# Optimization experiments

Measured on AMD Instinct MI355X. Metric: run time of the kernel, lower is better.

Reference implementation:

```python
import jax, jax.numpy as jnp
from jax import lax
import numpy as np

DN = ('NCHW', 'OIHW', 'NCHW')
EPS = 1e-8
LRELU_SLOPE = 0.2
SQRT2 = np.float32(np.sqrt(2.0))


def _blur2d(x):
    # 5x5 binomial FIR, depthwise, padding=2, stride=1 (Blur2d(kernel_size=5, padding=2))
    k1 = jnp.array([1.0, 4.0, 6.0, 4.0, 1.0], dtype=x.dtype)
    k2 = jnp.outer(k1, k1)
    k2 = k2 / k2.sum()
    C = x.shape[1]
    kern = jnp.broadcast_to(k2, (C, 1, 5, 5))
    return lax.conv_general_dilated(x, kern, window_strides=(1, 1),
                                    padding=[(2, 2), (2, 2)],
                                    feature_group_count=C,
                                    dimension_numbers=DN)


def _second_moment_norm(x, g):
    # normalize by per-channel spatial second moment, learnable gain g [C]
    ms = jnp.mean(jnp.square(x), axis=(2, 3), keepdims=True)  # [B,C,1,1]
    return x * lax.rsqrt(ms + EPS) * g[None, :, None, None]


def _modulated_conv(x, w, b, style_w, style_b, s, stride, padding):
    # StyleGAN2 modulated conv with demodulation, grouped-conv batch trick
    B, I, H, W = x.shape
    O, _, kh, kw = w.shape
    scale = np.float32(1.0 / np.sqrt(I * kh * kw))
    style = s @ style_w.T + style_b[None, :]                      # [B, I]
    wm = scale * w[None] * style[:, None, :, None, None]          # [B,O,I,kh,kw]
    d = lax.rsqrt(jnp.sum(jnp.square(wm), axis=(2, 3, 4)) + EPS)  # [B,O]
    wm = wm * d[:, :, None, None, None]
    xg = x.reshape(1, B * I, H, W)
    wg = wm.reshape(B * O, I, kh, kw)
    out = lax.conv_general_dilated(xg, wg, window_strides=(stride, stride),
                                   padding=[(padding, padding), (padding, padding)],
                                   feature_group_count=B,
                                   dimension_numbers=DN)
    out = out.reshape(B, O, out.shape[2], out.shape[3])
    return out + b[None, :, None, None]


def setup_inputs() -> dict:
    key = jax.random.key(0)
    ks = jax.random.split(key, 5)
    B, I, O, S, H, W, K = 8, 256, 256, 512, 128, 128, 3
    x = jax.random.normal(ks[0], (B, I, H, W), dtype=jnp.float32)
    s = jax.random.normal(ks[1], (B, S), dtype=jnp.float32)
    conv_w = jax.random.normal(ks[2], (O, I, K, K), dtype=jnp.float32)
    conv_b = jnp.zeros((O,), dtype=jnp.float32)
    style_w = jax.random.normal(ks[3], (I, S), dtype=jnp.float32) / np.float32(np.sqrt(S))
    style_b = jnp.ones((I,), dtype=jnp.float32)  # StyleGAN2 init: bias=1
    norm_g = jnp.ones((I,), dtype=jnp.float32)
    return {"x": x, "s": s, "conv_w": conv_w, "conv_b": conv_b,
            "style_w": style_w, "style_b": style_b, "norm_g": norm_g}


def reference(x, s, conv_w, conv_b, style_w, style_b, norm_g):
    x = _blur2d(x)                                   # blur (stride != 1 path)
    x = _second_moment_norm(x, norm_g)               # second-moment norm
    x = _modulated_conv(x, conv_w, conv_b, style_w, style_b, s, stride=2, padding=1)
    x = jnp.where(x >= 0, x, LRELU_SLOPE * x) * SQRT2  # scaled LeakyReLU
    return x
```

## Files before the change

kernel.cpp:

```cpp
#include <hip/hip_runtime.h>
#include <hip/hip_bf16.h>
#include <math.h>

#define B 8
#define IC 256
#define OC 256
#define SDIM 512
#define H 128
#define W 128
#define OH 64
#define OW 64
#define EPS 1e-8f
#define SQRT2 1.41421356237309504880f
#define SCALE 0.02083333395421505f

#define RS 16640
#define PLANE 1081600

typedef unsigned short u16;
typedef unsigned int u32;
typedef __attribute__((ext_vector_type(8))) short s16x8;
typedef __attribute__((ext_vector_type(4))) float f32x4;

__global__ void wsq_kernel(const float* __restrict__ w, float* __restrict__ wsq) {
    int i = blockIdx.x * 256 + threadIdx.x;
    const float* p = w + (size_t)i * 9;
    float sum = 0.f;
    for (int k = 0; k < 9; ++k) sum = fmaf(p[k], p[k], sum);
    wsq[i] = sum;
}

__global__ __launch_bounds__(256) void style_demod_kernel(const float* __restrict__ s,
                                                          const float* __restrict__ sw,
                                                          const float* __restrict__ sb,
                                                          const float* __restrict__ wsq,
                                                          float* __restrict__ style,
                                                          float* __restrict__ demod,
                                                          float* __restrict__ ssq) {
    __shared__ float st[256];
    const int b = blockIdx.x;
    const int tid = threadIdx.x;
    const float4* sv = (const float4*)(s + (size_t)b * SDIM);
    const float4* wv = (const float4*)(sw + (size_t)tid * SDIM);
    float sum = 0.f;
    #pragma unroll 4
    for (int k = 0; k < 128; ++k) {
        float4 a4 = sv[k], b4 = wv[k];
        sum = fmaf(a4.x, b4.x, fmaf(a4.y, b4.y, fmaf(a4.z, b4.z, fmaf(a4.w, b4.w, sum))));
    }
    float styv = sum + sb[tid];
    style[(b << 8) + tid] = styv;
    st[tid] = styv;
    ssq[(b << 8) + tid] = 0.f;
    __syncthreads();
    const float4* wq = (const float4*)(wsq + (size_t)tid * 256);
    float acc = 0.f;
    #pragma unroll 4
    for (int k = 0; k < 64; ++k) {
        float4 q = wq[k];
        float s0 = st[4 * k], s1 = st[4 * k + 1], s2 = st[4 * k + 2], s3 = st[4 * k + 3];
        acc = fmaf(s0 * s0, q.x, fmaf(s1 * s1, q.y, fmaf(s2 * s2, q.z, fmaf(s3 * s3, q.w, acc))));
    }
    demod[(b << 8) + tid] = rsqrtf(SCALE * SCALE * acc + EPS);
}

__global__ __launch_bounds__(256, 6) void blurpack_kernel(const float* __restrict__ x,
                                                          __hip_bfloat16* __restrict__ xbp,
                                                          float* __restrict__ ssq) {
    __shared__ __align__(16) char smem[24576];
    u16 (*raw)[12][128]  = reinterpret_cast<u16(*)[12][128]>(smem);
    u16 (*pbuf)[2][2][544] = reinterpret_cast<u16(*)[2][2][544]>(smem);
    const int t = threadIdx.x;
    const int strip = blockIdx.x;
    const int ic0 = blockIdx.y << 3;
    const int b = blockIdx.z;

    #pragma unroll
    for (int k = 0; k < 6; ++k) {
        int sidx = t + (k << 8);
        int r = sidx >> 7;
        int ch = (sidx >> 4) & 7;
        int cg = sidx & 15;
        int gr = (strip << 3) - 2 + r;
        uint4 q = {0u, 0u, 0u, 0u};
        if (gr >= 0 && gr < H) {
            const float* p = x + (((size_t)(b * 256 + ic0 + ch)) << 14) + (gr << 7) + (cg << 3);
            float4 v0 = *(const float4*)p;
            float4 v1 = *(const float4*)(p + 4);
            u16* qp = (u16*)&q;
            const float* vv0 = &v0.x;
            const float* vv1 = &v1.x;
            #pragma unroll
            for (int j = 0; j < 4; ++j) {
                __hip_bfloat16 b0 = __float2bfloat16(vv0[j]);
                __hip_bfloat16 b1 = __float2bfloat16(vv1[j]);
                qp[j] = *(u16*)&b0;
                qp[4 + j] = *(u16*)&b1;
            }
        }
        *(uint4*)&raw[ch][r][cg << 3] = q;
    }
    __syncthreads();

    const int hr = t >> 7;
    const int ch = (t >> 4) & 7;
    const int cg = t & 15;
    float ssacc = 0.f;
    uint2 res0[4], res1[4];

    #pragma unroll
    for (int pass = 0; pass < 4; ++pass) {
        const int br = (pass << 1) + hr;

        float v[8];
        {
            uint4 q0 = *(const uint4*)&raw[ch][br + 0][cg << 3];
            uint4 q1 = *(const uint4*)&raw[ch][br + 1][cg << 3];
            uint4 q2 = *(const uint4*)&raw[ch][br + 2][cg << 3];
            uint4 q3 = *(const uint4*)&raw[ch][br + 3][cg << 3];
            uint4 q4 = *(const uint4*)&raw[ch][br + 4][cg << 3];
            const u16* h0 = (const u16*)&q0; const u16* h1 = (const u16*)&q1;
            const u16* h2 = (const u16*)&q2; const u16* h3 = (const u16*)&q3;
            const u16* h4 = (const u16*)&q4;
            #pragma unroll
            for (int j = 0; j < 8; ++j) {
                float f0 = __uint_as_float(((u32)h0[j]) << 16);
                float f1 = __uint_as_float(((u32)h1[j]) << 16);
                float f2 = __uint_as_float(((u32)h2[j]) << 16);
                float f3 = __uint_as_float(((u32)h3[j]) << 16);
                float f4 = __uint_as_float(((u32)h4[j]) << 16);
                v[j] = fmaf(6.f, f2, fmaf(4.f, f1 + f3, f0 + f4));
            }
        }

        float vm2 = __shfl_up(v[6], 1, 64);
        float vm1 = __shfl_up(v[7], 1, 64);
        float vp1 = __shfl_down(v[0], 1, 64);
        float vp2 = __shfl_down(v[1], 1, 64);
        if (cg == 0)  { vm2 = 0.f; vm1 = 0.f; }
        if (cg == 15) { vp1 = 0.f; vp2 = 0.f; }
        float e[12];
        e[0] = vm2; e[1] = vm1;
        #pragma unroll
        for (int j = 0; j < 8; ++j) e[2 + j] = v[j];
        e[10] = vp1; e[11] = vp2;

        u16 hp[8];
        #pragma unroll
        for (int j = 0; j < 8; ++j) {
            float hv = fmaf(6.f, e[j + 2], fmaf(4.f, e[j + 1] + e[j + 3], e[j] + e[j + 4]))
                     * (1.0f / 256.0f);
            ssacc = fmaf(hv, hv, ssacc);
            __hip_bfloat16 hb = __float2bfloat16(hv);
            hp[j] = *(u16*)&hb;
        }
        u16 w0[4] = {hp[0], hp[2], hp[4], hp[6]};
        u16 w1[4] = {hp[1], hp[3], hp[5], hp[7]};
        res0[pass] = *(const uint2*)w0;
        res1[pass] = *(const uint2*)w1;
    }

    __syncthreads();

    #pragma unroll
    for (int pass = 0; pass < 4; ++pass) {
        *(uint2*)&pbuf[pass][hr][0][(ch << 6) + (cg << 2)] = res0[pass];
        *(uint2*)&pbuf[pass][hr][1][(ch << 6) + (cg << 2)] = res1[pass];
    }
    __syncthreads();

    {
        int fc = t & 127;
        int hr2 = t >> 7;
        int pw = fc & 1, pcol = fc >> 1;
        #pragma unroll
        for (int pass = 0; pass < 4; ++pass) {
            uint4 g;
            u16* gp = (u16*)&g;
            #pragma unroll
            for (int c2 = 0; c2 < 8; ++c2)
                gp[c2] = pbuf[pass][hr2][pw][(c2 << 6) + pcol];
            size_t off = (size_t)((b << 2) + (hr2 << 1) + pw) * PLANE
                       + (size_t)((strip << 2) + pass + 1) * RS
                       + (size_t)(pcol + 1) * 256 + ic0;
            *(uint4*)(xbp + off) = g;
        }
    }

    float sv2 = ssacc;
    sv2 += __shfl_down(sv2, 8, 16);
    sv2 += __shfl_down(sv2, 4, 16);
    sv2 += __shfl_down(sv2, 2, 16);
    sv2 += __shfl_down(sv2, 1, 16);
    if (cg == 0) atomicAdd(&ssq[(b << 8) + ic0 + ch], sv2);
}

__global__ void wf_kernel(const float* __restrict__ w,
                          const float* __restrict__ demod,
                          const float* __restrict__ ssq,
                          const float* __restrict__ style,
                          const float* __restrict__ g,
                          __hip_bfloat16* __restrict__ wf,
                          __hip_bfloat16* __restrict__ xbp) {
    int bo = blockIdx.x;
    int b = bo >> 8, o = bo & 255;
    int ic = threadIdx.x;
    float fac = rsqrtf(ssq[(b << 8) + ic] * (1.0f / 16384.0f) + EPS)
              * g[ic] * style[(b << 8) + ic] * SCALE;
    float m = demod[bo] * fac;
    const float* wp = w + ((size_t)o * 256 + ic) * 9;
    __hip_bfloat16* dst = wf + (size_t)bo * 2304 + ic;
    #pragma unroll
    for (int t = 0; t < 9; ++t)
        dst[t * 256] = __float2bfloat16(wp[t] * m);

    if (bo < 32) {
        int t = threadIdx.x;
        char* base = (char*)(xbp + (size_t)bo * PLANE);
        uint4 z = {0u, 0u, 0u, 0u};
        for (int k = 0; k < 9; ++k) {
            int c = t + (k << 8);
            if (c < 2080) *(uint4*)(base + (size_t)c * 16) = z;
        }
        for (int k = 0; k < 8; ++k) {
            int c = t + (k << 8);
            int r = 1 + (c >> 5);
            int off = (c & 31) << 3;
            *(uint4*)(base + ((size_t)r * RS + off) * 2) = z;
        }
    }
}

__device__ __forceinline__ void gl_lds16(const void* g, void* l) {
    __builtin_amdgcn_global_load_lds((const __attribute__((address_space(1))) u32*)g,
                                     (__attribute__((address_space(3))) u32*)l, 16, 0, 0);
}

__global__ __launch_bounds__(256, 2) void conv_kernel(const __hip_bfloat16* __restrict__ xbp,
                                                      const __hip_bfloat16* __restrict__ wf,
                                                      const float* __restrict__ bias,
                                                      float* __restrict__ out) {
    __shared__ char lds[65536];
    const int t = threadIdx.x;
    const int o0 = blockIdx.x << 7;
    const int y  = blockIdx.y;
    const int b  = blockIdx.z;
    const size_t bb = (size_t)b << 8;

    u32 aoffs[4], boffs[4];
    #pragma unroll
    for (int j = 0; j < 4; ++j) {
        int s = t + (j << 8);
        int r = s >> 3, m = s & 7;
        int g = m ^ (r & 7);
        aoffs[j] = (u32)(r * 2304 + (g << 3)) * 2;
        boffs[j] = (u32)((((y << 1) + (r >> 6)) * RS) + ((r & 63) << 8) + (g << 3)) * 2;
    }
    const char* gAbase = (const char*)(wf + (bb + o0) * 2304);

    const int lane = t & 63, wave = t >> 6;
    const int lr = lane & 15, quad = lane >> 4;
    const int mb = (wave & 1) << 6;
    const int nb = (wave >> 1) << 6;

    f32x4 acc[4][4];
    #pragma unroll
    for (int i = 0; i < 4; ++i)
        #pragma unroll
        for (int j = 0; j < 4; ++j) acc[i][j] = (f32x4){0.f, 0.f, 0.f, 0.f};

    #define STAGE_TILE(cc, bufbase)                                                        \
    {                                                                                      \
        int tap = (cc) >> 2;                                                               \
        int icq = ((cc) & 3) << 6;                                                         \
        int th = (tap * 11) >> 5;                                                          \
        int tw = tap - th * 3;                                                             \
        int ph  = (th == 1) ? 0 : 1;                                                       \
        int dhp = (th == 0) ? 0 : 1;                                                       \
        int pw  = (tw == 1) ? 0 : 1;                                                       \
        int dwp = (tw == 0) ? 0 : 1;                                                       \
        const char* gA = gAbase + (size_t)(tap * 256 + icq) * 2;                           \
        const char* gB = (const char*)(xbp + (size_t)((b << 2) + (ph << 1) + pw) * PLANE   \
                                       + (size_t)dhp * RS + (dwp << 8) + icq);             \
        char* dA = (bufbase) + t * 16;                                                     \
        char* dB = (bufbase) + 16384 + t * 16;                                             \
        _Pragma("unroll")                                                                  \
        for (int j = 0; j < 4; ++j) gl_lds16(gA + aoffs[j], dA + (j << 12));               \
        _Pragma("unroll")                                                                  \
        for (int j = 0; j < 4; ++j) gl_lds16(gB + boffs[j], dB + (j << 12));               \
    }

    STAGE_TILE(0, lds);
    __syncthreads();

    int cur = 0;
    for (int c = 0; c < 36; ++c) {
        if (c < 35) STAGE_TILE(c + 1, lds + ((cur ^ 1) << 15));

        const char* ldsA = lds + (cur << 15);
        const char* ldsB = ldsA + 16384;
        #pragma unroll
        for (int s = 0; s < 2; ++s) {
            const int mq = ((s << 2) + quad) ^ (lr & 7);
            s16x8 a[4], bf[4];
            #pragma unroll
            for (int i = 0; i < 4; ++i)
                a[i] = *(const s16x8*)(ldsA + ((mb + (i << 4) + lr) << 7) + (mq << 4));
            #pragma unroll
            for (int j = 0; j < 4; ++j)
                bf[j] = *(const s16x8*)(ldsB + ((nb + (j << 4) + lr) << 7) + (mq << 4));
            #pragma unroll
            for (int i = 0; i < 4; ++i)
                #pragma unroll
                for (int j = 0; j < 4; ++j)
                    acc[i][j] = __builtin_amdgcn_mfma_f32_16x16x32_bf16(a[i], bf[j], acc[i][j], 0, 0, 0);
        }
        __syncthreads();
        cur ^= 1;
    }
    #undef STAGE_TILE

    float bi[4][4];
    #pragma unroll
    for (int i = 0; i < 4; ++i)
        #pragma unroll
        for (int rr = 0; rr < 4; ++rr)
            bi[i][rr] = bias[o0 + mb + (i << 4) + (quad << 2) + rr];
    const int n0 = y << 7;
    #pragma unroll
    for (int i = 0; i < 4; ++i) {
        #pragma unroll
        for (int j = 0; j < 4; ++j) {
            #pragma unroll
            for (int rr = 0; rr < 4; ++rr) {
                int oc = o0 + mb + (i << 4) + (quad << 2) + rr;
                int n = n0 + nb + (j << 4) + lr;
                int oh = n >> 6, ow2 = n & 63;
                float v = acc[i][j][rr] + bi[i][rr];
                v = (v >= 0.f ? v : 0.2f * v) * SQRT2;
                out[((bb + oc) << 12) + (oh << 6) + ow2] = v;
            }
        }
    }
}

extern "C" void kernel_launch(void* const* d_in, const int* in_sizes, int n_in,
                              void* d_out, int out_size, void* d_ws, size_t ws_size,
                              hipStream_t stream) {
    const float* x   = (const float*)d_in[0];
    const float* s   = (const float*)d_in[1];
    const float* cw  = (const float*)d_in[2];
    const float* cb  = (const float*)d_in[3];
    const float* sw  = (const float*)d_in[4];
    const float* sb  = (const float*)d_in[5];
    const float* ng  = (const float*)d_in[6];
    float* out = (float*)d_out;

    char* ws = (char*)d_ws;
    __hip_bfloat16* xbp = (__hip_bfloat16*)ws;
    __hip_bfloat16* wfb = (__hip_bfloat16*)(ws + 69222400);
    float* style  = (float*)(ws + 78659584);
    float* wsq    = style + 2048;
    float* demod  = wsq + 65536;
    float* ssq    = demod + 2048;

    wsq_kernel<<<256, 256, 0, stream>>>(cw, wsq);
    style_demod_kernel<<<8, 256, 0, stream>>>(s, sw, sb, wsq, style, demod, ssq);
    blurpack_kernel<<<dim3(16, 32, 8), 256, 0, stream>>>(x, xbp, ssq);
    wf_kernel<<<2048, 256, 0, stream>>>(cw, demod, ssq, style, ng, wfb, xbp);
    conv_kernel<<<dim3(2, 32, 8), 256, 0, stream>>>(xbp, wfb, cb, out);
}
```

Before: 317.5 us.

## Halve blurpack strip height and remap conv blocks for XCD-local weight reuse

The blur/pack kernel now handles 4 output rows per block instead of 8, with twice as many blocks and a simpler float4-per-thread load of 8 input rows into a smaller LDS tile. This raises parallelism and lowers LDS use per block, at the cost of more halo re-reads. The conv kernel moves to a 1D grid whose block index is remapped so blocks sharing a batch and output-channel half run on the same XCD across rows. The goal is better L2 reuse of the modulated weights.

```diff
diff --git a/kernel.cpp b/kernel.cpp
--- a/kernel.cpp
+++ b/kernel.cpp
@@ -21,6 +21,11 @@
 typedef unsigned int u32;
 typedef __attribute__((ext_vector_type(8))) short s16x8;
 typedef __attribute__((ext_vector_type(4))) float f32x4;
+
+__device__ __forceinline__ void gl_lds16(const void* g, void* l) {
+    __builtin_amdgcn_global_load_lds((const __attribute__((address_space(1))) u32*)g,
+                                     (__attribute__((address_space(3))) u32*)l, 16, 0, 0);
+}
 
 __global__ void wsq_kernel(const float* __restrict__ w, float* __restrict__ wsq) {
     int i = blockIdx.x * 256 + threadIdx.x;
@@ -67,38 +72,35 @@
 __global__ __launch_bounds__(256, 6) void blurpack_kernel(const float* __restrict__ x,
                                                           __hip_bfloat16* __restrict__ xbp,
                                                           float* __restrict__ ssq) {
-    __shared__ __align__(16) char smem[24576];
-    u16 (*raw)[12][128]  = reinterpret_cast<u16(*)[12][128]>(smem);
+    __shared__ __align__(16) char smem[16384];
+    u16 (*raw)[8][128]    = reinterpret_cast<u16(*)[8][128]>(smem);
     u16 (*pbuf)[2][2][544] = reinterpret_cast<u16(*)[2][2][544]>(smem);
-    const int t = threadIdx.x;
     const int strip = blockIdx.x;
     const int ic0 = blockIdx.y << 3;
     const int b = blockIdx.z;
-
-    #pragma unroll
-    for (int k = 0; k < 6; ++k) {
-        int sidx = t + (k << 8);
-        int r = sidx >> 7;
-        int ch = (sidx >> 4) & 7;
-        int cg = sidx & 15;
-        int gr = (strip << 3) - 2 + r;
-        uint4 q = {0u, 0u, 0u, 0u};
-        if (gr >= 0 && gr < H) {
-            const float* p = x + (((size_t)(b * 256 + ic0 + ch)) << 14) + (gr << 7) + (cg << 3);
-            float4 v0 = *(const float4*)p;
-            float4 v1 = *(const float4*)(p + 4);
-            u16* qp = (u16*)&q;
-            const float* vv0 = &v0.x;
-            const float* vv1 = &v1.x;
+    const int t = threadIdx.x;
+
+    {
+        const int sch = t >> 5, g = t & 31;
+        const float* xch = x + (((size_t)(b * 256 + ic0 + sch)) << 14) + (g << 2);
+        float4 vals[8];
+        #pragma unroll
+        for (int k = 0; k < 8; ++k) {
+            int gr = (strip << 2) - 2 + k;
+            if (gr >= 0 && gr < H) vals[k] = *(const float4*)(xch + ((size_t)gr << 7));
+            else                   vals[k] = (float4){0.f, 0.f, 0.f, 0.f};
+        }
+        #pragma unroll
+        for (int k = 0; k < 8; ++k) {
+            u16 h[4];
+            const float* vv = &vals[k].x;
             #pragma unroll
             for (int j = 0; j < 4; ++j) {
-                __hip_bfloat16 b0 = __float2bfloat16(vv0[j]);
-                __hip_bfloat16 b1 = __float2bfloat16(vv1[j]);
-                qp[j] = *(u16*)&b0;
-                qp[4 + j] = *(u16*)&b1;
+                __hip_bfloat16 hb = __float2bfloat16(vv[j]);
+                h[j] = *(u16*)&hb;
             }
-        }
-        *(uint4*)&raw[ch][r][cg << 3] = q;
+            *(uint2*)&raw[sch][k][g << 2] = *(const uint2*)h;
+        }
     }
     __syncthreads();
 
@@ -106,10 +108,10 @@
     const int ch = (t >> 4) & 7;
     const int cg = t & 15;
     float ssacc = 0.f;
-    uint2 res0[4], res1[4];
-
-    #pragma unroll
-    for (int pass = 0; pass < 4; ++pass) {
+    uint2 res0[2], res1[2];
+
+    #pragma unroll
+    for (int pass = 0; pass < 2; ++pass) {
         const int br = (pass << 1) + hr;
 
         float v[8];
@@ -163,7 +165,7 @@
     __syncthreads();
 
     #pragma unroll
-    for (int pass = 0; pass < 4; ++pass) {
+    for (int pass = 0; pass < 2; ++pass) {
         *(uint2*)&pbuf[pass][hr][0][(ch << 6) + (cg << 2)] = res0[pass];
         *(uint2*)&pbuf[pass][hr][1][(ch << 6) + (cg << 2)] = res1[pass];
     }
@@ -174,14 +176,14 @@
         int hr2 = t >> 7;
         int pw = fc & 1, pcol = fc >> 1;
         #pragma unroll
-        for (int pass = 0; pass < 4; ++pass) {
+        for (int pass = 0; pass < 2; ++pass) {
             uint4 g;
             u16* gp = (u16*)&g;
             #pragma unroll
             for (int c2 = 0; c2 < 8; ++c2)
                 gp[c2] = pbuf[pass][hr2][pw][(c2 << 6) + pcol];
             size_t off = (size_t)((b << 2) + (hr2 << 1) + pw) * PLANE
-                       + (size_t)((strip << 2) + pass + 1) * RS
+                       + (size_t)((strip << 1) + pass + 1) * RS
                        + (size_t)(pcol + 1) * 256 + ic0;
             *(uint4*)(xbp + off) = g;
         }
@@ -231,20 +233,18 @@
     }
 }
 
-__device__ __forceinline__ void gl_lds16(const void* g, void* l) {
-    __builtin_amdgcn_global_load_lds((const __attribute__((address_space(1))) u32*)g,
-                                     (__attribute__((address_space(3))) u32*)l, 16, 0, 0);
-}
-
 __global__ __launch_bounds__(256, 2) void conv_kernel(const __hip_bfloat16* __restrict__ xbp,
                                                       const __hip_bfloat16* __restrict__ wf,
                                                       const float* __restrict__ bias,
                                                       float* __restrict__ out) {
     __shared__ char lds[65536];
     const int t = threadIdx.x;
-    const int o0 = blockIdx.x << 7;
-    const int y  = blockIdx.y;
-    const int b  = blockIdx.z;
+    const int bid = blockIdx.x;
+    const int xcd = bid & 7;
+    const int y   = (bid >> 3) & 31;
+    const int p   = xcd + (((bid >> 8) & 1) << 3);
+    const int o0  = (p & 1) << 7;
+    const int b   = p >> 1;
     const size_t bb = (size_t)b << 8;
 
     u32 aoffs[4], boffs[4];
@@ -366,7 +366,7 @@
 
     wsq_kernel<<<256, 256, 0, stream>>>(cw, wsq);
     style_demod_kernel<<<8, 256, 0, stream>>>(s, sw, sb, wsq, style, demod, ssq);
-    blurpack_kernel<<<dim3(16, 32, 8), 256, 0, stream>>>(x, xbp, ssq);
+    blurpack_kernel<<<dim3(32, 32, 8), 256, 0, stream>>>(x, xbp, ssq);
     wf_kernel<<<2048, 256, 0, stream>>>(cw, demod, ssq, style, ng, wfb, xbp);
-    conv_kernel<<<dim3(2, 32, 8), 256, 0, stream>>>(xbp, wfb, cb, out);
-}
+    conv_kernel<<<512, 256, 0, stream>>>(xbp, wfb, cb, out);
+}
```

Measured after the change: 320.2 us. No clear change (+0.9%).
